# Kernel tuning notes

Hardware: AMD Instinct MI355X
Metric: run time of the kernel (lower is better)

The kernel has to match this reference:

```python
import jax, jax.numpy as jnp
import numpy as np

DIM = 256
HEADS = 8
W0, W1 = 8, 8
N = W0 * W1
SCALE = (DIM // HEADS) ** (-0.5)


def _rel_pos_index(w0, w1):
    ch = np.arange(w0)
    cw = np.arange(w1)
    coords = np.stack(np.meshgrid(ch, cw, indexing='ij')).reshape(2, -1)  # (2, N)
    rel = coords[:, :, None] - coords[:, None, :]                          # (2, N, N)
    rel = rel.transpose(1, 2, 0).copy()                                    # (N, N, 2)
    rel[:, :, 0] += w0 - 1
    rel[:, :, 1] += w1 - 1
    rel[:, :, 0] *= 2 * w1 - 1
    return rel.sum(-1)                                                     # (N, N)

REL_IDX = jnp.asarray(_rel_pos_index(W0, W1))


def setup_inputs() -> dict:
    key = jax.random.key(0)
    ks = jax.random.split(key, 9)
    B, C, H, W = 8, DIM, 128, 128
    s = DIM ** -0.5
    return {
        'x': jax.random.normal(ks[0], (B, C, H, W), jnp.float32),
        'embedding': jax.random.normal(ks[1], (1, N, DIM), jnp.float32),
        'rpb_table': jax.random.normal(ks[2], ((2 * W0 - 1) * (2 * W1 - 1), HEADS), jnp.float32),
        'q_w': jax.random.normal(ks[3], (DIM, DIM), jnp.float32) * s,
        'q_b': jnp.zeros((DIM,), jnp.float32),
        'kv_w': jax.random.normal(ks[4], (2 * DIM, DIM), jnp.float32) * s,
        'kv_b': jnp.zeros((2 * DIM,), jnp.float32),
        'proj_w': jax.random.normal(ks[5], (DIM, DIM), jnp.float32) * s,
        'proj_b': jnp.zeros((DIM,), jnp.float32),
    }


def reference(x, embedding, rpb_table, q_w, q_b, kv_w, kv_b, proj_w, proj_b):
    B, C, H, W = x.shape
    # window_partition (faithful to the original, incl. its discarded-permute view):
    # torch views the contiguous (B,C,H,W) buffer as (B, H//w0, w0, W//w1, w1, C)
    win = x.reshape(B, H // W0, W0, W // W1, W1, C)
    win = win.transpose(0, 1, 3, 2, 4, 5).reshape(-1, N, C)  # (Bw, N, C)
    Bw = win.shape[0]
    hd = C // HEADS

    q = jnp.einsum('bnc,dc->bnd', jnp.broadcast_to(embedding, (Bw, N, C)), q_w) + q_b
    q = q.reshape(Bw, N, HEADS, hd).transpose(0, 2, 1, 3)      # (Bw, h, N, hd)
    kv = jnp.einsum('bnc,dc->bnd', win, kv_w) + kv_b           # (Bw, N, 2C)
    kv = kv.reshape(Bw, N, 2, HEADS, hd).transpose(2, 0, 3, 1, 4)
    k, v = kv[0], kv[1]                                         # (Bw, h, N, hd)

    bias = rpb_table[REL_IDX.reshape(-1)].reshape(N, N, HEADS).transpose(2, 0, 1)  # (h, N, N)

    attn = jnp.einsum('bhnd,bhmd->bhnm', q * SCALE, k) + bias[None]
    attn = jax.nn.softmax(attn, axis=-1)
    out = jnp.einsum('bhnm,bhmd->bhnd', attn, v)
    out = out.transpose(0, 2, 1, 3).reshape(Bw, N, C)
    out = jnp.einsum('bnc,dc->bnd', out, proj_w) + proj_b
    return out
```

## Files before the change

kernel.cpp:

```cpp
#include <hip/hip_runtime.h>

typedef short bf16x8 __attribute__((ext_vector_type(8)));
typedef float f32x4 __attribute__((ext_vector_type(4)));
typedef float f32x16 __attribute__((ext_vector_type(16)));
typedef unsigned u32;
typedef unsigned short u16;
typedef unsigned u32x4v __attribute__((ext_vector_type(4)));
typedef unsigned u32x2v __attribute__((ext_vector_type(2)));

union UV { u32x4v u; bf16x8 v; };

__device__ __forceinline__ u16 f2bf(float f){
  u32 u = __float_as_uint(f);
  u += 0x7FFFu + ((u>>16)&1u);
  return (u16)(u>>16);
}
__device__ __forceinline__ u32 pack2(float lo, float hi){
  return (u32)f2bf(lo) | ((u32)f2bf(hi)<<16);
}

__global__ void k_qs(const float* __restrict__ emb, const float* __restrict__ q_w,
                     const float* __restrict__ q_b, u16* __restrict__ q_s){
  const int n = blockIdx.x;
  const int d = threadIdx.x;
  const float4* er = (const float4*)(emb + n*256);
  const float4* wr = (const float4*)(q_w + d*256);
  float acc = 0.f;
  for(int c=0;c<64;++c){
    float4 e = er[c], w = wr[c];
    acc += e.x*w.x + e.y*w.y + e.z*w.z + e.w*w.w;
  }
  acc += q_b[d];
  q_s[n*256 + d] = f2bf(acc * 0.17677669529663687f);
}

__global__ void k_bias(const float* __restrict__ rpb, float* __restrict__ bias){
  const int o = blockIdx.x*256 + threadIdx.x;
  const int h = o>>12, n = (o>>6)&63, m = o&63;
  const int idx = ((n>>3)-(m>>3)+7)*15 + ((n&7)-(m&7)+7);
  bias[o] = rpb[idx*8 + h];
}

__global__ void k_wcvt(const float* __restrict__ kv_w, const float* __restrict__ proj_w,
                       u32* __restrict__ kvb, u32* __restrict__ pjb){
  const int i = blockIdx.x*256 + threadIdx.x;
  if(i < 65536) kvb[i] = pack2(kv_w[2*i], kv_w[2*i+1]);
  else { int j = i - 65536; pjb[j] = pack2(proj_w[2*j], proj_w[2*j+1]); }
}

__global__ __launch_bounds__(512,4) void k_fused(const float* __restrict__ x, const u16* __restrict__ kvw,
                                                 const float* __restrict__ kv_b, const u16* __restrict__ q_s,
                                                 const float* __restrict__ bias, const u16* __restrict__ pjw,
                                                 const float* __restrict__ proj_b, float* __restrict__ out){
  __shared__ char R1[32768];

  const int bw = blockIdx.x;
  const int b = bw>>8, h1 = (bw>>4)&15, w1 = bw&15;
  const int base = b*4194304 + h1*262144 + w1*2048;
  const int tid = threadIdx.x;
  const int w = tid>>6, l = tid&63, g = l>>4, li = l&15;
  const int l31 = l&31, hi = l>>5;

  #pragma unroll
  for(int i=0;i<4;++i){
    int p = i*512 + tid;
    int n = p>>5;
    int c4 = (2*p)&63;
    const float4* gp = (const float4*)(x + base + (n>>3)*32768 + (n&7)*256 + c4*4);
    float4 lo = gp[0], hh = gp[1];
    u32x4v d = { pack2(lo.x,lo.y), pack2(lo.z,lo.w), pack2(hh.x,hh.y), pack2(hh.z,hh.w) };
    *(u32x4v*)(R1 + ((p*16) ^ ((n&7)<<4)));
    *(u32x4v*)(R1 + ((p*16) ^ ((n&7)<<4))) = d;
  }
  __syncthreads();

  f32x4 acc[4][4];
  #pragma unroll
  for(int ct=0;ct<4;++ct){
    float bv = kv_b[w*64 + ct*16 + li];
    #pragma unroll
    for(int rt=0;rt<4;++rt) acc[rt][ct] = (f32x4){bv,bv,bv,bv};
  }
  for(int ks=0;ks<8;++ks){
    bf16x8 a[4];
    #pragma unroll
    for(int rt=0;rt<4;++rt){
      int n = rt*16 + li;
      a[rt] = *(const bf16x8*)(R1 + ((n*512 + ks*64 + g*16) ^ ((n&7)<<4)));
    }
    #pragma unroll
    for(int ct=0;ct<4;++ct){
      bf16x8 bfr = *(const bf16x8*)(kvw + (w*64 + ct*16 + li)*256 + ks*32 + g*8);
      #pragma unroll
      for(int rt=0;rt<4;++rt)
        acc[rt][ct] = __builtin_amdgcn_mfma_f32_16x16x32_bf16(a[rt], bfr, acc[rt][ct], 0,0,0);
    }
  }
  __syncthreads();

  const int h = w;
  bf16x8 qf[2][2];
  #pragma unroll
  for(int nt=0;nt<2;++nt)
    #pragma unroll
    for(int ks=0;ks<2;++ks)
      qf[nt][ks] = *(const bf16x8*)(q_s + (nt*32 + l31)*256 + h*32 + ks*16 + hi*8);

  if(w < 4){
    #pragma unroll
    for(int ct=0;ct<4;++ct){
      int col = w*64 + ct*16 + li;
      #pragma unroll
      for(int rt=0;rt<4;++rt)
        #pragma unroll
        for(int r=0;r<4;++r){
          int row = rt*16 + 4*g + r;
          *(u16*)(R1 + ((row*512 + col*2) ^ ((row&7)<<4))) = f2bf(acc[rt][ct][r]);
        }
    }
  }
  __syncthreads();

  bf16x8 kf[2][2];
  #pragma unroll
  for(int mt=0;mt<2;++mt)
    #pragma unroll
    for(int ks=0;ks<2;++ks){
      int row = mt*32 + l31;
      kf[mt][ks] = *(const bf16x8*)(R1 + ((row*512 + (h*32 + ks*16 + hi*8)*2) ^ ((row&7)<<4)));
    }
  __syncthreads();

  if(w >= 4){
    #pragma unroll
    for(int ct=0;ct<4;++ct){
      int c2 = (w-4)*64 + ct*16 + li;
      int hv = c2>>5, e = c2&31;
      #pragma unroll
      for(int rt=0;rt<4;++rt){
        u32x2v d;
        d[0] = pack2(acc[rt][ct][0], acc[rt][ct][1]);
        d[1] = pack2(acc[rt][ct][2], acc[rt][ct][3]);
        int m0 = rt*16 + 4*g;
        *(u32x2v*)(R1 + (((hv*32 + e)*128 + m0*2) ^ ((e&7)<<4))) = d;
      }
    }
  }
  __syncthreads();

  f32x16 S[2][2];
  #pragma unroll
  for(int mt=0;mt<2;++mt)
    #pragma unroll
    for(int nt=0;nt<2;++nt){
      int n = nt*32 + l31;
      const float* bp = bias + h*4096 + n*64 + mt*32 + 4*hi;
      #pragma unroll
      for(int q=0;q<4;++q){
        float4 bv = *(const float4*)(bp + q*8);
        S[mt][nt][4*q+0] = bv.x; S[mt][nt][4*q+1] = bv.y;
        S[mt][nt][4*q+2] = bv.z; S[mt][nt][4*q+3] = bv.w;
      }
    }
  #pragma unroll
  for(int ks=0;ks<2;++ks)
    #pragma unroll
    for(int mt=0;mt<2;++mt)
      #pragma unroll
      for(int nt=0;nt<2;++nt)
        S[mt][nt] = __builtin_amdgcn_mfma_f32_32x32x16_bf16(kf[mt][ks], qf[nt][ks], S[mt][nt], 0,0,0);

  float rs[2];
  u32 cb0[2][8], cb1[2][8];
  #pragma unroll
  for(int nt=0;nt<2;++nt){
    float t[16];
    #pragma unroll
    for(int j=0;j<16;++j) t[j] = fmaxf(S[0][nt][j], S[1][nt][j]);
    #pragma unroll
    for(int s=8;s>0;s>>=1)
      #pragma unroll
      for(int j=0;j<8;++j) if(j<s) t[j] = fmaxf(t[j], t[j+s]);
    float mx = fmaxf(t[0], __shfl_xor(t[0], 32));
    float sm[16];
    #pragma unroll
    for(int j=0;j<16;++j){
      S[0][nt][j] = __expf(S[0][nt][j] - mx);
      S[1][nt][j] = __expf(S[1][nt][j] - mx);
      sm[j] = S[0][nt][j] + S[1][nt][j];
    }
    #pragma unroll
    for(int s=8;s>0;s>>=1)
      #pragma unroll
      for(int j=0;j<8;++j) if(j<s) sm[j] += sm[j+s];
    float total = sm[0] + __shfl_xor(sm[0], 32);
    rs[nt] = 1.0f/total;
    #pragma unroll
    for(int mt=0;mt<2;++mt)
      #pragma unroll
      for(int q=0;q<4;++q){
        cb0[nt][mt*4+q] = pack2(S[mt][nt][4*q+0], S[mt][nt][4*q+1]);
        cb1[nt][mt*4+q] = pack2(S[mt][nt][4*q+2], S[mt][nt][4*q+3]);
      }
  }

  f32x16 O[2];
  O[0] = (f32x16)(0.f); O[1] = (f32x16)(0.f);
  #pragma unroll
  for(int ks2=0;ks2<4;++ks2){
    bf16x8 vf = *(const bf16x8*)(R1 + (((h*32 + l31)*128 + (ks2*16 + hi*8)*2) ^ ((l31&7)<<4)));
    #pragma unroll
    for(int nt=0;nt<2;++nt){
      u32 A0 = cb0[nt][2*ks2], B0 = cb0[nt][2*ks2+1];
      u32 A1 = cb1[nt][2*ks2], B1 = cb1[nt][2*ks2+1];
      u32 r0 = (u32)__shfl_xor((int)(hi ? A0 : B0), 32);
      u32 r1 = (u32)__shfl_xor((int)(hi ? A1 : B1), 32);
      u32 w0 = hi ? r0 : A0;
      u32 w1 = hi ? r1 : A1;
      u32 w2 = hi ? B0 : r0;
      u32 w3 = hi ? B1 : r1;
      UV t; t.u = (u32x4v){w0,w1,w2,w3};
      O[nt] = __builtin_amdgcn_mfma_f32_32x32x16_bf16(vf, t.v, O[nt], 0,0,0);
    }
  }

  #pragma unroll
  for(int nt=0;nt<2;++nt){
    int n = nt*32 + l31;
    #pragma unroll
    for(int q=0;q<4;++q){
      u32x2v d;
      d[0] = pack2(O[nt][4*q+0]*rs[nt], O[nt][4*q+1]*rs[nt]);
      d[1] = pack2(O[nt][4*q+2]*rs[nt], O[nt][4*q+3]*rs[nt]);
      *(u32x2v*)(R1 + h*4096 + ((n*64 + (8*q + 4*hi)*2) ^ ((n&7)<<4))) = d;
    }
  }
  __syncthreads();

  {
    f32x4 pacc[4][2];
    #pragma unroll
    for(int ct=0;ct<2;++ct){
      float bv = proj_b[w*32 + ct*16 + li];
      #pragma unroll
      for(int rt=0;rt<4;++rt) pacc[rt][ct] = (f32x4){bv,bv,bv,bv};
    }
    for(int ks=0;ks<8;++ks){
      bf16x8 a[4];
      #pragma unroll
      for(int rt=0;rt<4;++rt){
        int row = rt*16 + li;
        a[rt] = *(const bf16x8*)(R1 + ks*4096 + ((row*64 + g*16) ^ ((row&7)<<4)));
      }
      #pragma unroll
      for(int ct=0;ct<2;++ct){
        bf16x8 bfr = *(const bf16x8*)(pjw + (w*32 + ct*16 + li)*256 + ks*32 + g*8);
        #pragma unroll
        for(int rt=0;rt<4;++rt)
          pacc[rt][ct] = __builtin_amdgcn_mfma_f32_16x16x32_bf16(a[rt], bfr, pacc[rt][ct], 0,0,0);
      }
    }
    #pragma unroll
    for(int rt=0;rt<4;++rt)
      #pragma unroll
      for(int ct=0;ct<2;++ct)
        #pragma unroll
        for(int r=0;r<4;++r)
          out[(bw*64 + rt*16 + 4*g + r)*256 + w*32 + ct*16 + li] = pacc[rt][ct][r];
  }
}

extern "C" void kernel_launch(void* const* d_in, const int* in_sizes, int n_in,
                              void* d_out, int out_size, void* d_ws, size_t ws_size,
                              hipStream_t stream){
  (void)in_sizes; (void)n_in; (void)out_size;
  const float* x      = (const float*)d_in[0];
  const float* emb    = (const float*)d_in[1];
  const float* rpb    = (const float*)d_in[2];
  const float* q_w    = (const float*)d_in[3];
  const float* q_b    = (const float*)d_in[4];
  const float* kv_w   = (const float*)d_in[5];
  const float* kv_b   = (const float*)d_in[6];
  const float* proj_w = (const float*)d_in[7];
  const float* proj_b = (const float*)d_in[8];
  float* out = (float*)d_out;

  char* ws = (char*)d_ws;
  if(ws_size < (size_t)557056) return;
  u16* q_s   = (u16*)(ws);
  float* bias= (float*)(ws + 32768);
  u32* kvb   = (u32*)(ws + 163840);
  u32* pjb   = (u32*)(ws + 425984);

  k_qs   <<<  64, 256, 0, stream>>>(emb, q_w, q_b, q_s);
  k_bias <<< 128, 256, 0, stream>>>(rpb, bias);
  k_wcvt <<< 384, 256, 0, stream>>>(kv_w, proj_w, kvb, pjb);
  k_fused<<<2048, 512, 0, stream>>>(x, (const u16*)kvb, kv_b, q_s, bias,
                                    (const u16*)pjb, proj_b, out);
}
```

Baseline: 364.7 us.

## Prefetch weight fragments, use hardware bf16 pack, exp2 softmax, paired LDS stores

Several micro-optimizations land together. The KV and projection GEMM loops are fully unrolled and load the next k-step's weight fragment from global memory while the current MFMAs run. Float-to-bf16 packing now uses the v_cvt_pk_bf16_f32 instruction instead of manual rounding. Softmax uses exp2, with the log2e factor folded into the Q scale and the bias. The K store to LDS swaps values between neighbouring lanes so each lane writes 32-bit pairs instead of 16-bit scalars. These raise register pressure and add lane shuffles in exchange for less load latency and fewer instructions.

```diff
diff --git a/kernel.cpp b/kernel.cpp
--- a/kernel.cpp
+++ b/kernel.cpp
@@ -16,8 +16,12 @@
   return (u16)(u>>16);
 }
 __device__ __forceinline__ u32 pack2(float lo, float hi){
-  return (u32)f2bf(lo) | ((u32)f2bf(hi)<<16);
-}
+  u32 r;
+  asm("v_cvt_pk_bf16_f32 %0, %1, %2" : "=v"(r) : "v"(lo), "v"(hi));
+  return r;
+}
+
+#define LOG2E 1.4426950408889634f
 
 __global__ void k_qs(const float* __restrict__ emb, const float* __restrict__ q_w,
                      const float* __restrict__ q_b, u16* __restrict__ q_s){
@@ -31,14 +35,14 @@
     acc += e.x*w.x + e.y*w.y + e.z*w.z + e.w*w.w;
   }
   acc += q_b[d];
-  q_s[n*256 + d] = f2bf(acc * 0.17677669529663687f);
+  q_s[n*256 + d] = f2bf(acc * (0.17677669529663687f * LOG2E));
 }
 
 __global__ void k_bias(const float* __restrict__ rpb, float* __restrict__ bias){
   const int o = blockIdx.x*256 + threadIdx.x;
   const int h = o>>12, n = (o>>6)&63, m = o&63;
   const int idx = ((n>>3)-(m>>3)+7)*15 + ((n&7)-(m&7)+7);
-  bias[o] = rpb[idx*8 + h];
+  bias[o] = rpb[idx*8 + h] * LOG2E;
 }
 
 __global__ void k_wcvt(const float* __restrict__ kv_w, const float* __restrict__ proj_w,
@@ -69,7 +73,6 @@
     const float4* gp = (const float4*)(x + base + (n>>3)*32768 + (n&7)*256 + c4*4);
     float4 lo = gp[0], hh = gp[1];
     u32x4v d = { pack2(lo.x,lo.y), pack2(lo.z,lo.w), pack2(hh.x,hh.y), pack2(hh.z,hh.w) };
-    *(u32x4v*)(R1 + ((p*16) ^ ((n&7)<<4)));
     *(u32x4v*)(R1 + ((p*16) ^ ((n&7)<<4))) = d;
   }
   __syncthreads();
@@ -81,19 +84,26 @@
     #pragma unroll
     for(int rt=0;rt<4;++rt) acc[rt][ct] = (f32x4){bv,bv,bv,bv};
   }
-  for(int ks=0;ks<8;++ks){
-    bf16x8 a[4];
-    #pragma unroll
-    for(int rt=0;rt<4;++rt){
-      int n = rt*16 + li;
-      a[rt] = *(const bf16x8*)(R1 + ((n*512 + ks*64 + g*16) ^ ((n&7)<<4)));
-    }
-    #pragma unroll
-    for(int ct=0;ct<4;++ct){
-      bf16x8 bfr = *(const bf16x8*)(kvw + (w*64 + ct*16 + li)*256 + ks*32 + g*8);
-      #pragma unroll
-      for(int rt=0;rt<4;++rt)
-        acc[rt][ct] = __builtin_amdgcn_mfma_f32_16x16x32_bf16(a[rt], bfr, acc[rt][ct], 0,0,0);
+  {
+    const u16* wbase = kvw + (w*64 + li)*256 + g*8;
+    bf16x8 bcur[4];
+    #pragma unroll
+    for(int ct=0;ct<4;++ct) bcur[ct] = *(const bf16x8*)(wbase + ct*4096);
+    #pragma unroll
+    for(int ks=0;ks<8;++ks){
+      bf16x8 a[4];
+      #pragma unroll
+      for(int rt=0;rt<4;++rt){
+        int n = rt*16 + li;
+        a[rt] = *(const bf16x8*)(R1 + ((n*512 + ks*64 + g*16) ^ ((n&7)<<4)));
+      }
+      #pragma unroll
+      for(int ct=0;ct<4;++ct){
+        #pragma unroll
+        for(int rt=0;rt<4;++rt)
+          acc[rt][ct] = __builtin_amdgcn_mfma_f32_16x16x32_bf16(a[rt], bcur[ct], acc[rt][ct], 0,0,0);
+        if(ks<7) bcur[ct] = *(const bf16x8*)(wbase + ct*4096 + (ks+1)*32);
+      }
     }
   }
   __syncthreads();
@@ -106,17 +116,21 @@
     for(int ks=0;ks<2;++ks)
       qf[nt][ks] = *(const bf16x8*)(q_s + (nt*32 + l31)*256 + h*32 + ks*16 + hi*8);
 
+  const int oddl = li & 1;
   if(w < 4){
     #pragma unroll
     for(int ct=0;ct<4;++ct){
-      int col = w*64 + ct*16 + li;
-      #pragma unroll
-      for(int rt=0;rt<4;++rt)
-        #pragma unroll
-        for(int r=0;r<4;++r){
-          int row = rt*16 + 4*g + r;
-          *(u16*)(R1 + ((row*512 + col*2) ^ ((row&7)<<4))) = f2bf(acc[rt][ct][r]);
-        }
+      int colp = w*64 + ct*16 + (li & ~1);
+      #pragma unroll
+      for(int rt=0;rt<4;++rt){
+        float v0=acc[rt][ct][0], v1=acc[rt][ct][1], v2=acc[rt][ct][2], v3=acc[rt][ct][3];
+        float o0=__shfl_xor(v0,1), o1=__shfl_xor(v1,1), o2=__shfl_xor(v2,1), o3=__shfl_xor(v3,1);
+        u32 d0 = oddl ? pack2(o2,v2) : pack2(v0,o0);
+        u32 d1 = oddl ? pack2(o3,v3) : pack2(v1,o1);
+        int row0 = rt*16 + 4*g + (oddl ? 2 : 0);
+        *(u32*)(R1 + ((row0*512     + colp*2) ^ ((row0&7)<<4)))     = d0;
+        *(u32*)(R1 + (((row0+1)*512 + colp*2) ^ (((row0+1)&7)<<4))) = d1;
+      }
     }
   }
   __syncthreads();
@@ -185,8 +199,8 @@
     float sm[16];
     #pragma unroll
     for(int j=0;j<16;++j){
-      S[0][nt][j] = __expf(S[0][nt][j] - mx);
-      S[1][nt][j] = __expf(S[1][nt][j] - mx);
+      S[0][nt][j] = __builtin_amdgcn_exp2f(S[0][nt][j] - mx);
+      S[1][nt][j] = __builtin_amdgcn_exp2f(S[1][nt][j] - mx);
       sm[j] = S[0][nt][j] + S[1][nt][j];
     }
     #pragma unroll
@@ -245,6 +259,11 @@
       #pragma unroll
       for(int rt=0;rt<4;++rt) pacc[rt][ct] = (f32x4){bv,bv,bv,bv};
     }
+    const u16* pbase = pjw + (w*32 + li)*256 + g*8;
+    bf16x8 bc[2];
+    #pragma unroll
+    for(int ct=0;ct<2;++ct) bc[ct] = *(const bf16x8*)(pbase + ct*4096);
+    #pragma unroll
     for(int ks=0;ks<8;++ks){
       bf16x8 a[4];
       #pragma unroll
@@ -254,10 +273,10 @@
       }
       #pragma unroll
       for(int ct=0;ct<2;++ct){
-        bf16x8 bfr = *(const bf16x8*)(pjw + (w*32 + ct*16 + li)*256 + ks*32 + g*8);
         #pragma unroll
         for(int rt=0;rt<4;++rt)
-          pacc[rt][ct] = __builtin_amdgcn_mfma_f32_16x16x32_bf16(a[rt], bfr, pacc[rt][ct], 0,0,0);
+          pacc[rt][ct] = __builtin_amdgcn_mfma_f32_16x16x32_bf16(a[rt], bc[ct], pacc[rt][ct], 0,0,0);
+        if(ks<7) bc[ct] = *(const bf16x8*)(pbase + ct*4096 + (ks+1)*32);
       }
     }
     #pragma unroll
```

After: 360.5 us. About the same (-1.2%).
